# Performance work log

Hardware: AMD Instinct MI355X
Metric: run time of the kernel (lower is better)

## Reference

```python
import jax, jax.numpy as jnp
import numpy as np

B, L, D, W = 4, 512, 768, 12
K = L * W  # number of candidate spans


def _mlp(x, w1, b1, w2, b2):
    # Linear -> ReLU -> (Dropout=identity in eval) -> Linear
    return jax.nn.relu(x @ w1.T + b1) @ w2.T + b2


def setup_inputs() -> dict:
    key = jax.random.key(0)
    ks = jax.random.split(key, 16)
    sc_d = 1.0 / np.sqrt(D)
    sc_4d = 1.0 / np.sqrt(4 * D)
    sc_2d = 1.0 / np.sqrt(2 * D)
    inp = {
        "h": jax.random.normal(ks[0], (B, L, D), dtype=jnp.float32),
        "span_idx": jax.random.randint(ks[1], (B, K, 2), 0, L, dtype=jnp.int64),
        # project_start: Linear(D,4D), Linear(4D,D)
        "ws1": jax.random.uniform(ks[2], (4 * D, D), jnp.float32, -sc_d, sc_d),
        "bs1": jax.random.uniform(ks[3], (4 * D,), jnp.float32, -sc_d, sc_d),
        "ws2": jax.random.uniform(ks[4], (D, 4 * D), jnp.float32, -sc_4d, sc_4d),
        "bs2": jax.random.uniform(ks[5], (D,), jnp.float32, -sc_4d, sc_4d),
        # project_end
        "we1": jax.random.uniform(ks[6], (4 * D, D), jnp.float32, -sc_d, sc_d),
        "be1": jax.random.uniform(ks[7], (4 * D,), jnp.float32, -sc_d, sc_d),
        "we2": jax.random.uniform(ks[8], (D, 4 * D), jnp.float32, -sc_4d, sc_4d),
        "be2": jax.random.uniform(ks[9], (D,), jnp.float32, -sc_4d, sc_4d),
        # out_project: Linear(2D,4D), Linear(4D,D)
        "wo1": jax.random.uniform(ks[10], (4 * D, 2 * D), jnp.float32, -sc_2d, sc_2d),
        "bo1": jax.random.uniform(ks[11], (4 * D,), jnp.float32, -sc_2d, sc_2d),
        "wo2": jax.random.uniform(ks[12], (D, 4 * D), jnp.float32, -sc_4d, sc_4d),
        "bo2": jax.random.uniform(ks[13], (D,), jnp.float32, -sc_4d, sc_4d),
    }
    return inp


def reference(h, span_idx, ws1, bs1, ws2, bs2, we1, be1, we2, be2, wo1, bo1, wo2, bo2):
    start_rep = _mlp(h, ws1, bs1, ws2, bs2)  # [B, L, D]
    end_rep = _mlp(h, we1, be1, we2, be2)    # [B, L, D]
    bidx = jnp.arange(B)[:, None]
    start_span = start_rep[bidx, span_idx[:, :, 0]]  # gather along seq dim -> [B, K, D]
    end_span = end_rep[bidx, span_idx[:, :, 1]]      # [B, K, D]
    cat = jax.nn.relu(jnp.concatenate([start_span, end_span], axis=-1))  # [B, K, 2D]
    out = _mlp(cat, wo1, bo1, wo2, bo2)  # [B, K, D]
    return out.reshape(B, L, W, D)
```

## Files before the change

### kernel.cpp

```cpp
#include <hip/hip_runtime.h>
#include <hip/hip_bf16.h>

using bf16 = __hip_bfloat16;
using bf16x8 = __attribute__((ext_vector_type(8))) __bf16;
using f32x4  = __attribute__((ext_vector_type(4))) float;
typedef unsigned short ushort_t;

#define BM 128
#define BN 128
#define BK 32


__device__ __forceinline__ void gl_lds16(const void* g, void* l) {
  __builtin_amdgcn_global_load_lds(
      (const __attribute__((address_space(1))) void*)g,
      (__attribute__((address_space(3))) void*)l, 16, 0, 0);
}

__device__ __forceinline__ ushort_t f2bf(float f) {
  unsigned u = __float_as_uint(f);
  u += 0x7FFF + ((u >> 16) & 1);
  return (ushort_t)(u >> 16);
}

__global__ void sniff(const unsigned* __restrict__ w1,
                      const unsigned* __restrict__ idx, int* flags) {
  __shared__ int cnt[2];
  if (threadIdx.x == 0) { cnt[0] = 0; cnt[1] = 0; }
  __syncthreads();
  int t = threadIdx.x;
  int c0 = 0;
  for (int k = 0; k < 4; ++k) {
    unsigned lo = w1[t * 4 + k] & 0xFFFFu;
    unsigned e = (lo >> 7) & 0xFF;
    if (e <= 122) c0++;
  }
  int c1 = (idx[2 * t + 1] != 0) ? 1 : 0;
  atomicAdd(&cnt[0], c0);
  atomicAdd(&cnt[1], c1);
  __syncthreads();
  if (threadIdx.x == 0) {
    flags[0] = (cnt[0] >= 900) ? 1 : 0;
    flags[1] = (cnt[1] == 0) ? 1 : 0;
  }
}

__global__ void norm_idx(const int* __restrict__ flags, const void* __restrict__ src,
                         int* __restrict__ dst) {
  int i = blockIdx.x * 256 + threadIdx.x;
  int v = flags[1] ? (int)((const long long*)src)[i] : ((const int*)src)[i];
  dst[i] = v;
}

__global__ void cvt_all(const int* __restrict__ flags,
                        const void* s0, const void* s1, const void* s2,
                        const void* s3, const void* s4, const void* s5,
                        const void* s6, ushort_t* __restrict__ dst) {
  long i = ((long)blockIdx.x * 256 + threadIdx.x) * 4;
  const void* src; long off;
  if      (i <  1572864) { src = s0; off = i; }
  else if (i <  3932160) { src = s1; off = i - 1572864; }
  else if (i <  6291456) { src = s2; off = i - 3932160; }
  else if (i <  8650752) { src = s3; off = i - 6291456; }
  else if (i < 11010048) { src = s4; off = i - 8650752; }
  else if (i < 15728640) { src = s5; off = i - 11010048; }
  else                   { src = s6; off = i - 15728640; }
  if (flags[0]) {
    *(ushort4*)(dst + i) = *((const ushort4*)((const ushort_t*)src + off));
  } else {
    float4 f = ((const float4*)src)[off >> 2];
    ushort4 o;
    o.x = f2bf(f.x); o.y = f2bf(f.y); o.z = f2bf(f.z); o.w = f2bf(f.w);
    *(ushort4*)(dst + i) = o;
  }
}

__global__ void cvt_bias(const int* __restrict__ flags,
                         const void* b0, const void* b1, const void* b2,
                         const void* b3, const void* b4, const void* b5,
                         float* __restrict__ dst) {
  int i = blockIdx.x * 256 + threadIdx.x;
  if (i >= 14592) return;
  if (i >= 11520) { dst[i] = 0.f; return; }
  const void* src; int off;
  if (i < 3072)       { src = b0; off = i; }
  else if (i < 3840)  { src = b1; off = i - 3072; }
  else if (i < 6912)  { src = b2; off = i - 3840; }
  else if (i < 7680)  { src = b3; off = i - 6912; }
  else if (i < 10752) { src = b4; off = i - 7680; }
  else                { src = b5; off = i - 10752; }
  dst[i] = flags[0] ? __bfloat162float(((const bf16*)src)[off])
                    : ((const float*)src)[off];
}

template <bool GATHER, bool RELU, bool OUTF32>
__global__ __launch_bounds__(256) void gemm_bt(
    const bf16* __restrict__ A, const bf16* __restrict__ A2,
    const bf16* __restrict__ repS, const bf16* __restrict__ repE,
    const int* __restrict__ sidx, int row_base,
    const bf16* __restrict__ Bw, const bf16* __restrict__ Bw2,
    const float* __restrict__ bias, const float* __restrict__ bias2,
    void* __restrict__ C, void* __restrict__ C2, int nsplit,
    int N, int Kdim, int bstride) {
  __shared__ bf16 lA[BM * BK];
  __shared__ bf16 lB[BN * BK];

  const int tid  = threadIdx.x;
  const int lane = tid & 63;
  const int wave = tid >> 6;
  const int wm = wave >> 1, wn = wave & 1;
  int by = blockIdx.y;
  const bf16* Bw_ = Bw; const float* bias_ = bias; void* C_ = C; const bf16* A_ = A;
  if (by >= nsplit) { by -= nsplit; Bw_ = Bw2; bias_ = bias2; C_ = C2; A_ = A2; }
  const int m0 = blockIdx.x * BM;
  const int n0 = by * BN;

  const int srow = tid >> 2;
  const int scol = 8 * ((tid & 3) ^ ((tid >> 3) & 3));

  const bf16 *a0 = nullptr, *a1 = nullptr;
  const bf16 *pS0 = nullptr, *pE0 = nullptr, *pS1 = nullptr, *pE1 = nullptr;
  if (GATHER) {
    int r0 = row_base + m0 + srow;
    int r1 = r0 + 64;
    int b0 = r0 / 6144, b1 = r1 / 6144;
    int s0 = min(max(sidx[2 * r0], 0), 511);
    int e0 = min(max(sidx[2 * r0 + 1], 0), 511);
    int s1 = min(max(sidx[2 * r1], 0), 511);
    int e1 = min(max(sidx[2 * r1 + 1], 0), 511);
    pS0 = repS + ((size_t)b0 * 512 + s0) * 768 + scol;
    pE0 = repE + ((size_t)b0 * 512 + e0) * 768 + scol;
    pS1 = repS + ((size_t)b1 * 512 + s1) * 768 + scol;
    pE1 = repE + ((size_t)b1 * 512 + e1) * 768 + scol;
  } else {
    a0 = A_ + (size_t)(m0 + srow) * Kdim + scol;
    a1 = a0 + (size_t)64 * Kdim;
  }
  const bf16* b0p = Bw_ + (size_t)(n0 + srow) * bstride + scol;
  const bf16* b1p = b0p + (size_t)64 * bstride;

  f32x4 acc[4][4];
  const f32x4 z = {0.f, 0.f, 0.f, 0.f};
#pragma unroll
  for (int i = 0; i < 4; ++i)
#pragma unroll
    for (int j = 0; j < 4; ++j) acc[i][j] = z;

  const int fr = lane & 15;
  const int fk = 8 * ((lane >> 4) ^ ((lane >> 1) & 3));

  for (int k0 = 0; k0 < Kdim; k0 += BK) {
    const bf16 *sa0, *sa1;
    if (GATHER) {
      if (k0 < 768) { sa0 = pS0 + k0; sa1 = pS1 + k0; }
      else          { sa0 = pE0 + (k0 - 768); sa1 = pE1 + (k0 - 768); }
    } else {
      sa0 = a0 + k0; sa1 = a1 + k0;
    }
    gl_lds16(sa0, lA + tid * 8);
    gl_lds16(sa1, lA + 2048 + tid * 8);
    gl_lds16(b0p + k0, lB + tid * 8);
    gl_lds16(b1p + k0, lB + 2048 + tid * 8);
    __syncthreads();

    bf16x8 af[4], bv[4];
#pragma unroll
    for (int i = 0; i < 4; ++i)
      af[i] = *(const bf16x8*)(const void*)(lA + (wm * 64 + i * 16 + fr) * BK + fk);
#pragma unroll
    for (int j = 0; j < 4; ++j)
      bv[j] = *(const bf16x8*)(const void*)(lB + (wn * 64 + j * 16 + fr) * BK + fk);
#pragma unroll
    for (int i = 0; i < 4; ++i)
#pragma unroll
      for (int j = 0; j < 4; ++j)
        acc[i][j] = __builtin_amdgcn_mfma_f32_16x16x32_bf16(af[i], bv[j], acc[i][j], 0, 0, 0);
    __syncthreads();
  }

  float* Cf = (float*)C_;
  bf16*  Cb = (bf16*)C_;
#pragma unroll
  for (int j = 0; j < 4; ++j) {
    int n = n0 + wn * 64 + j * 16 + fr;
    float bj = bias_[n];
#pragma unroll
    for (int i = 0; i < 4; ++i) {
      int mb = m0 + wm * 64 + i * 16 + (lane >> 4) * 4;
#pragma unroll
      for (int r = 0; r < 4; ++r) {
        float v = acc[i][j][r] + bj;
        if (RELU) v = fmaxf(v, 0.f);
        if (OUTF32) Cf[(size_t)(mb + r) * N + n] = v;
        else        Cb[(size_t)(mb + r) * N + n] = __float2bfloat16(v);
      }
    }
  }
}

#define FM 64
#define FN 128
__global__ __launch_bounds__(256) void gemm_final_fused(
    const ushort_t* __restrict__ Ps, const ushort_t* __restrict__ Pe,
    const int* __restrict__ sidx,
    const bf16* __restrict__ Bw, const float* __restrict__ bias,
    float* __restrict__ out) {
  __shared__ bf16 lA[2 * 2048];
  __shared__ bf16 lB[2 * 4096];

  const int tid  = threadIdx.x;
  const int lane = tid & 63;
  const int wave = tid >> 6;
  const int wm = wave >> 1, wn = wave & 1;
  const int m0 = blockIdx.x * FM;
  const int n0 = blockIdx.y * FN;

  const int srow = tid >> 2;
  const int scol = 8 * ((tid & 3) ^ ((tid >> 3) & 3));

  int r0 = m0 + srow;
  int b0 = r0 / 6144;
  int s0 = min(max(sidx[2 * r0], 0), 511);
  int e0 = min(max(sidx[2 * r0 + 1], 0), 511);
  const ushort_t* pS0 = Ps + ((size_t)b0 * 512 + s0) * 3072 + scol;
  const ushort_t* pE0 = Pe + ((size_t)b0 * 512 + e0) * 3072 + scol;

  const bf16* bp0 = Bw + (size_t)(n0 + srow) * 3072 + scol;
  const bf16* bp1 = bp0 + (size_t)64 * 3072;

  f32x4 acc[2][4];
  const f32x4 z = {0.f, 0.f, 0.f, 0.f};
#pragma unroll
  for (int i = 0; i < 2; ++i)
#pragma unroll
    for (int j = 0; j < 4; ++j) acc[i][j] = z;

  const int fr = lane & 15;
  const int fk = 8 * ((lane >> 4) ^ ((lane >> 1) & 3));

  auto pack_store = [&](uint4 xs, uint4 xe, bf16* dst) {
    unsigned w[4];
    const unsigned* us = &xs.x;
    const unsigned* ue = &xe.x;
#pragma unroll
    for (int q = 0; q < 4; ++q) {
      float lo = fmaxf(__uint_as_float(us[q] << 16) + __uint_as_float(ue[q] << 16), 0.f);
      float hi = fmaxf(__uint_as_float(us[q] & 0xFFFF0000u) +
                       __uint_as_float(ue[q] & 0xFFFF0000u), 0.f);
      asm("v_cvt_pk_bf16_f32 %0, %1, %2" : "=v"(w[q]) : "v"(lo), "v"(hi));
    }
    *(uint4*)(void*)dst = *(const uint4*)w;
  };

  {
    gl_lds16(bp0, lB + tid * 8);
    gl_lds16(bp1, lB + 2048 + tid * 8);
    uint4 xs0 = *(const uint4*)(const void*)pS0;
    uint4 xe0 = *(const uint4*)(const void*)pE0;
    pack_store(xs0, xe0, lA + tid * 8);
    __syncthreads();
  }

  for (int it = 0; it < 96; ++it) {
    const int curA = (it & 1) << 11;
    const int curB = (it & 1) << 12;
    const int nxtA = ((it + 1) & 1) << 11;
    const int nxtB = ((it + 1) & 1) << 12;
    const int k1 = (it + 1) * BK;
    const bool pre = (it + 1) < 96;
    uint4 xs0, xe0;
    if (pre) {
      gl_lds16(bp0 + k1, lB + nxtB + tid * 8);
      gl_lds16(bp1 + k1, lB + nxtB + 2048 + tid * 8);
      xs0 = *(const uint4*)(const void*)(pS0 + k1);
      xe0 = *(const uint4*)(const void*)(pE0 + k1);
    }

    bf16x8 af[2];
#pragma unroll
    for (int i = 0; i < 2; ++i)
      af[i] = *(const bf16x8*)(const void*)(lA + curA + (wm * 32 + i * 16 + fr) * BK + fk);
#pragma unroll
    for (int j = 0; j < 4; ++j) {
      bf16x8 bv = *(const bf16x8*)(const void*)(lB + curB + (wn * 64 + j * 16 + fr) * BK + fk);
#pragma unroll
      for (int i = 0; i < 2; ++i)
        acc[i][j] = __builtin_amdgcn_mfma_f32_16x16x32_bf16(af[i], bv, acc[i][j], 0, 0, 0);
    }

    if (pre) {
      pack_store(xs0, xe0, lA + nxtA + tid * 8);
    }
    __syncthreads();
  }

#pragma unroll
  for (int j = 0; j < 4; ++j) {
    int n = n0 + wn * 64 + j * 16 + fr;
    float bj = bias[n];
#pragma unroll
    for (int i = 0; i < 2; ++i) {
      int mb = m0 + wm * 32 + i * 16 + (lane >> 4) * 4;
#pragma unroll
      for (int r = 0; r < 4; ++r)
        out[(size_t)(mb + r) * 768 + n] = acc[i][j][r] + bj;
    }
  }
}

extern "C" void kernel_launch(void* const* d_in, const int* in_sizes, int n_in,
                              void* d_out, int out_size, void* d_ws, size_t ws_size,
                              hipStream_t stream) {
  const void* h    = d_in[0];
  const void* sidx = d_in[1];
  const void *ws1 = d_in[2],  *bs1 = d_in[3];
  const void *ws2 = d_in[4],  *bs2 = d_in[5];
  const void *we1 = d_in[6],  *be1 = d_in[7];
  const void *we2 = d_in[8],  *be2 = d_in[9];
  const void *wo1 = d_in[10], *bo1 = d_in[11];
  const void *wo2 = d_in[12], *bo2 = d_in[13];

  char* p = (char*)d_ws;
  int*      flags = (int*)p;
  int*      idx32 = (int*)(p + 256);
  float*    biasf = (float*)(p + 256 + 196608);
  ushort_t* hb    = (ushort_t*)(p + 256 + 196608 + 65536);
  ushort_t* w1sb  = hb   + (size_t)1572864;
  ushort_t* w2sb  = w1sb + (size_t)2359296;
  ushort_t* w1eb  = w2sb + (size_t)2359296;
  ushort_t* w2eb  = w1eb + (size_t)2359296;
  ushort_t* wo1b  = w2eb + (size_t)2359296;
  ushort_t* wo2b  = wo1b + (size_t)4718592;
  ushort_t* repS  = wo2b + (size_t)2359296;
  ushort_t* repE  = repS + (size_t)1572864;
  char*     R     = (char*)(repE + (size_t)1572864);
  size_t fixed = (size_t)(R - (char*)d_ws);
  if (ws_size < fixed) return;
  size_t Rsz = ws_size - fixed;

  const size_t P_BF = (size_t)2 * 2048 * 3072 * 2;
  int tier = (Rsz >= P_BF) ? 2 : 3;

  dim3 blk(256);
  const int XBIG = 0x40000000;
  sniff<<<1, blk, 0, stream>>>((const unsigned*)ws1, (const unsigned*)sidx, flags);
  norm_idx<<<192, blk, 0, stream>>>(flags, sidx, idx32);
  cvt_all<<<17664, blk, 0, stream>>>(flags, h, ws1, ws2, we1, we2, wo1, wo2, hb);
  cvt_bias<<<57, blk, 0, stream>>>(flags, bs1, bs2, be1, be2, bo1, bo2, biasf);
  const float *bs1f = biasf, *bs2f = biasf + 3072, *be1f = biasf + 3840,
              *be2f = biasf + 6912, *bo1f = biasf + 7680, *bo2f = biasf + 10752,
              *zerof = biasf + 11520;
  float* outf = (float*)d_out;

  if (tier == 2) {
    ushort_t* hidS = (ushort_t*)R;
    ushort_t* hidE = hidS + (size_t)2048 * 3072;
    gemm_bt<false, true, false><<<dim3(16, 48), blk, 0, stream>>>(
        (const bf16*)hb, (const bf16*)hb, nullptr, nullptr, nullptr, 0,
        (const bf16*)w1sb, (const bf16*)w1eb, bs1f, be1f,
        hidS, hidE, 24, 3072, 768, 768);
    gemm_bt<false, true, false><<<dim3(16, 12), blk, 0, stream>>>(
        (const bf16*)hidS, (const bf16*)hidE, nullptr, nullptr, nullptr, 0,
        (const bf16*)w2sb, (const bf16*)w2eb, bs2f, be2f,
        (bf16*)repS, (bf16*)repE, 6, 768, 3072, 3072);
    ushort_t* Ps = (ushort_t*)R;
    ushort_t* Pe = Ps + (size_t)2048 * 3072;
    gemm_bt<false, false, false><<<dim3(16, 48), blk, 0, stream>>>(
        (const bf16*)repS, (const bf16*)repE, nullptr, nullptr, nullptr, 0,
        (const bf16*)wo1b, (const bf16*)wo1b + 768, bo1f, zerof,
        Ps, Pe, 24, 3072, 768, 1536);
    gemm_final_fused<<<dim3(384, 6), blk, 0, stream>>>(
        Ps, Pe, idx32, (const bf16*)wo2b, bo2f, outf);
  } else {
    long long cT = (long long)(Rsz / ((size_t)2 * 3072 * 2));
    cT = (cT / 128) * 128; if (cT > 2048) cT = 2048;
    long long cO = (long long)(Rsz / ((size_t)3072 * 2));
    cO = (cO / 128) * 128; if (cO > 24576) cO = 24576;
    if (cT < 128 || cO < 128) return;
    ushort_t* scr = (ushort_t*)R;
    for (long long r = 0; r < 2048; r += cT) {
      long long mc = 2048 - r < cT ? 2048 - r : cT;
      ushort_t* hidS = scr;
      ushort_t* hidE = scr + (size_t)cT * 3072;
      gemm_bt<false, true, false><<<dim3(mc / 128, 48), blk, 0, stream>>>(
          (const bf16*)hb + r * 768, (const bf16*)hb + r * 768,
          nullptr, nullptr, nullptr, 0,
          (const bf16*)w1sb, (const bf16*)w1eb, bs1f, be1f,
          hidS, hidE, 24, 3072, 768, 768);
      gemm_bt<false, true, false><<<dim3(mc / 128, 12), blk, 0, stream>>>(
          (const bf16*)hidS, (const bf16*)hidE, nullptr, nullptr, nullptr, 0,
          (const bf16*)w2sb, (const bf16*)w2eb, bs2f, be2f,
          (bf16*)repS + r * 768, (bf16*)repE + r * 768, 6, 768, 3072, 3072);
    }
    for (long long r = 0; r < 24576; r += cO) {
      long long mc = 24576 - r < cO ? 24576 - r : cO;
      gemm_bt<true, true, false><<<dim3(mc / 128, 24), blk, 0, stream>>>(
          nullptr, nullptr, (const bf16*)repS, (const bf16*)repE, idx32, (int)r,
          (const bf16*)wo1b, nullptr, bo1f, nullptr,
          scr, nullptr, XBIG, 3072, 1536, 1536);
      gemm_bt<false, false, true><<<dim3(mc / 128, 6), blk, 0, stream>>>(
          (const bf16*)scr, nullptr, nullptr, nullptr, nullptr, 0,
          (const bf16*)wo2b, nullptr, bo2f, nullptr,
          outf + (size_t)r * 768, nullptr, XBIG, 768, 3072, 3072);
    }
  }
}
```

Measured before the change: 562.6 us.

## Deepen A-operand prefetch to two stages with explicit waitcnt scheduling

Restructures the final out-projection GEMM main loop so the gathered start/end span rows are loaded two K-steps ahead in registers, while the weight tile is still loaded one step ahead via global_load_lds. Scheduling barriers and manual vmcnt/lgkmcnt waits replace __syncthreads. This lets the gather latency overlap more MFMA work instead of stalling. It costs extra registers for the second prefetch buffer, and the hand-written wait counts depend on the exact issue order, so the pipeline is fragile.

```diff
diff --git a/kernel.cpp b/kernel.cpp
--- a/kernel.cpp
+++ b/kernel.cpp
@@ -4,6 +4,7 @@
 using bf16 = __hip_bfloat16;
 using bf16x8 = __attribute__((ext_vector_type(8))) __bf16;
 using f32x4  = __attribute__((ext_vector_type(4))) float;
+using u32x4  = __attribute__((ext_vector_type(4))) unsigned;
 typedef unsigned short ushort_t;
 
 #define BM 128
@@ -16,6 +17,10 @@
       (const __attribute__((address_space(1))) void*)g,
       (__attribute__((address_space(3))) void*)l, 16, 0, 0);
 }
+
+#define SB0() __builtin_amdgcn_sched_barrier(0)
+#define WAITV(n) asm volatile("s_waitcnt vmcnt(" #n ")" ::: "memory")
+#define WAITL() asm volatile("s_waitcnt lgkmcnt(0)" ::: "memory")
 
 __device__ __forceinline__ ushort_t f2bf(float f) {
   unsigned u = __float_as_uint(f);
@@ -238,61 +243,93 @@
   const int fr = lane & 15;
   const int fk = 8 * ((lane >> 4) ^ ((lane >> 1) & 3));
 
-  auto pack_store = [&](uint4 xs, uint4 xe, bf16* dst) {
-    unsigned w[4];
-    const unsigned* us = &xs.x;
-    const unsigned* ue = &xe.x;
+  auto pack_store = [&](u32x4 xs, u32x4 xe, bf16* dst) {
+    u32x4 wv;
 #pragma unroll
     for (int q = 0; q < 4; ++q) {
-      float lo = fmaxf(__uint_as_float(us[q] << 16) + __uint_as_float(ue[q] << 16), 0.f);
-      float hi = fmaxf(__uint_as_float(us[q] & 0xFFFF0000u) +
-                       __uint_as_float(ue[q] & 0xFFFF0000u), 0.f);
-      asm("v_cvt_pk_bf16_f32 %0, %1, %2" : "=v"(w[q]) : "v"(lo), "v"(hi));
-    }
-    *(uint4*)(void*)dst = *(const uint4*)w;
+      float lo = fmaxf(__uint_as_float(xs[q] << 16) + __uint_as_float(xe[q] << 16), 0.f);
+      float hi = fmaxf(__uint_as_float(xs[q] & 0xFFFF0000u) +
+                       __uint_as_float(xe[q] & 0xFFFF0000u), 0.f);
+      unsigned w;
+      asm("v_cvt_pk_bf16_f32 %0, %1, %2" : "=v"(w) : "v"(lo), "v"(hi));
+      wv[q] = w;
+    }
+    *(u32x4*)(void*)dst = wv;
   };
 
-  {
-    gl_lds16(bp0, lB + tid * 8);
-    gl_lds16(bp1, lB + 2048 + tid * 8);
-    uint4 xs0 = *(const uint4*)(const void*)pS0;
-    uint4 xe0 = *(const uint4*)(const void*)pE0;
-    pack_store(xs0, xe0, lA + tid * 8);
-    __syncthreads();
-  }
-
-  for (int it = 0; it < 96; ++it) {
-    const int curA = (it & 1) << 11;
-    const int curB = (it & 1) << 12;
-    const int nxtA = ((it + 1) & 1) << 11;
-    const int nxtB = ((it + 1) & 1) << 12;
-    const int k1 = (it + 1) * BK;
-    const bool pre = (it + 1) < 96;
-    uint4 xs0, xe0;
-    if (pre) {
-      gl_lds16(bp0 + k1, lB + nxtB + tid * 8);
-      gl_lds16(bp1 + k1, lB + nxtB + 2048 + tid * 8);
-      xs0 = *(const uint4*)(const void*)(pS0 + k1);
-      xe0 = *(const uint4*)(const void*)(pE0 + k1);
-    }
-
+  auto mfma_tile = [&](int cA, int cB) {
     bf16x8 af[2];
 #pragma unroll
     for (int i = 0; i < 2; ++i)
-      af[i] = *(const bf16x8*)(const void*)(lA + curA + (wm * 32 + i * 16 + fr) * BK + fk);
+      af[i] = *(const bf16x8*)(const void*)(lA + cA + (wm * 32 + i * 16 + fr) * BK + fk);
 #pragma unroll
     for (int j = 0; j < 4; ++j) {
-      bf16x8 bv = *(const bf16x8*)(const void*)(lB + curB + (wn * 64 + j * 16 + fr) * BK + fk);
+      bf16x8 bv = *(const bf16x8*)(const void*)(lB + cB + (wn * 64 + j * 16 + fr) * BK + fk);
 #pragma unroll
       for (int i = 0; i < 2; ++i)
         acc[i][j] = __builtin_amdgcn_mfma_f32_16x16x32_bf16(af[i], bv, acc[i][j], 0, 0, 0);
     }
-
-    if (pre) {
-      pack_store(xs0, xe0, lA + nxtA + tid * 8);
-    }
-    __syncthreads();
-  }
+  };
+
+  u32x4 xs0, xe0, xs1, xe1;
+
+  xs0 = *(const u32x4*)(const void*)pS0;
+  xe0 = *(const u32x4*)(const void*)pE0;
+  SB0();
+  gl_lds16(bp0, lB + tid * 8);
+  gl_lds16(bp1, lB + 2048 + tid * 8);
+  SB0();
+  xs1 = *(const u32x4*)(const void*)(pS0 + 32);
+  xe1 = *(const u32x4*)(const void*)(pE0 + 32);
+  SB0();
+  pack_store(xs0, xe0, lA + tid * 8);
+  WAITV(2);
+  WAITL();
+  SB0();
+  __builtin_amdgcn_s_barrier();
+  SB0();
+
+  auto kstep = [&](int t, u32x4& sPk, u32x4& ePk, u32x4& sLd, u32x4& eLd) {
+    const int cA = (t & 1) << 11, cB = (t & 1) << 12;
+    const int nA = cA ^ 2048,     nB = cB ^ 4096;
+    const int kB = (t + 1) * BK;
+    const int kA = (t + 2) * BK;
+    gl_lds16(bp0 + kB, lB + nB + tid * 8);
+    gl_lds16(bp1 + kB, lB + nB + 2048 + tid * 8);
+    SB0();
+    sLd = *(const u32x4*)(const void*)(pS0 + kA);
+    eLd = *(const u32x4*)(const void*)(pE0 + kA);
+    SB0();
+
+    mfma_tile(cA, cB);
+
+    pack_store(sPk, ePk, lA + nA + tid * 8);
+    WAITV(2);
+    WAITL();
+    SB0();
+    __builtin_amdgcn_s_barrier();
+    SB0();
+  };
+
+  for (int m = 0; m < 47; ++m) {
+    kstep(2 * m,     xs1, xe1, xs0, xe0);
+    kstep(2 * m + 1, xs0, xe0, xs1, xe1);
+  }
+
+  {
+    gl_lds16(bp0 + 95 * BK, lB + 4096 + tid * 8);
+    gl_lds16(bp1 + 95 * BK, lB + 4096 + 2048 + tid * 8);
+    SB0();
+    mfma_tile(0, 0);
+    pack_store(xs1, xe1, lA + 2048 + tid * 8);
+    WAITV(0);
+    WAITL();
+    SB0();
+    __builtin_amdgcn_s_barrier();
+    SB0();
+  }
+
+  mfma_tile(2048, 4096);
 
 #pragma unroll
   for (int j = 0; j < 4; ++j) {
```

New measurement: 557.2 us. Within noise of the previous version (-1.0%).

## Widen final fused GEMM tile to 64x384 with 8 waves to cut gather redundancy

Applied to the files above, without the earlier changes.

The final gather+GEMM kernel now uses 512-thread blocks, each computing a 64x384 output tile instead of 64x128. The grid shrinks from 6 to 2 column blocks. Each gathered Ps/Pe row pair is then loaded and ReLU-packed only twice instead of six times, which cuts redundant gather traffic and ALU work. The cost is a larger LDS footprint for B (about 48KB double-buffered), half the threads idle during A packing, and fewer blocks in flight per CU.

```diff
diff --git a/kernel.cpp b/kernel.cpp
--- a/kernel.cpp
+++ b/kernel.cpp
@@ -4,6 +4,7 @@
 using bf16 = __hip_bfloat16;
 using bf16x8 = __attribute__((ext_vector_type(8))) __bf16;
 using f32x4  = __attribute__((ext_vector_type(4))) float;
+using u32x4  = __attribute__((ext_vector_type(4))) unsigned;
 typedef unsigned short ushort_t;
 
 #define BM 128
@@ -198,109 +199,117 @@
   }
 }
 
-#define FM 64
-#define FN 128
-__global__ __launch_bounds__(256) void gemm_final_fused(
+__global__ __launch_bounds__(512) void gemm_final_fused(
     const ushort_t* __restrict__ Ps, const ushort_t* __restrict__ Pe,
     const int* __restrict__ sidx,
     const bf16* __restrict__ Bw, const float* __restrict__ bias,
     float* __restrict__ out) {
   __shared__ bf16 lA[2 * 2048];
-  __shared__ bf16 lB[2 * 4096];
+  __shared__ bf16 lB[2 * 12288];
 
   const int tid  = threadIdx.x;
   const int lane = tid & 63;
   const int wave = tid >> 6;
-  const int wm = wave >> 1, wn = wave & 1;
-  const int m0 = blockIdx.x * FM;
-  const int n0 = blockIdx.y * FN;
+  const int m0 = blockIdx.x * 64;
+  const int n0 = blockIdx.y * 384;
 
   const int srow = tid >> 2;
   const int scol = 8 * ((tid & 3) ^ ((tid >> 3) & 3));
 
-  int r0 = m0 + srow;
-  int b0 = r0 / 6144;
-  int s0 = min(max(sidx[2 * r0], 0), 511);
-  int e0 = min(max(sidx[2 * r0 + 1], 0), 511);
-  const ushort_t* pS0 = Ps + ((size_t)b0 * 512 + s0) * 3072 + scol;
-  const ushort_t* pE0 = Pe + ((size_t)b0 * 512 + e0) * 3072 + scol;
-
-  const bf16* bp0 = Bw + (size_t)(n0 + srow) * 3072 + scol;
-  const bf16* bp1 = bp0 + (size_t)64 * 3072;
-
-  f32x4 acc[2][4];
+  const ushort_t *pS0 = nullptr, *pE0 = nullptr;
+  if (tid < 256) {
+    int r0 = m0 + srow;
+    int b0 = r0 / 6144;
+    int s0 = min(max(sidx[2 * r0], 0), 511);
+    int e0 = min(max(sidx[2 * r0 + 1], 0), 511);
+    pS0 = Ps + ((size_t)b0 * 512 + s0) * 3072 + scol;
+    pE0 = Pe + ((size_t)b0 * 512 + e0) * 3072 + scol;
+  }
+  const bf16* bp0 = Bw + (size_t)(n0 +       srow) * 3072 + scol;
+  const bf16* bp1 = Bw + (size_t)(n0 + 128 + srow) * 3072 + scol;
+  const bf16* bp2 = Bw + (size_t)(n0 + 256 + srow) * 3072 + scol;
+
+  f32x4 acc[4][3];
   const f32x4 z = {0.f, 0.f, 0.f, 0.f};
 #pragma unroll
-  for (int i = 0; i < 2; ++i)
-#pragma unroll
-    for (int j = 0; j < 4; ++j) acc[i][j] = z;
+  for (int i = 0; i < 4; ++i)
+#pragma unroll
+    for (int j = 0; j < 3; ++j) acc[i][j] = z;
 
   const int fr = lane & 15;
   const int fk = 8 * ((lane >> 4) ^ ((lane >> 1) & 3));
 
-  auto pack_store = [&](uint4 xs, uint4 xe, bf16* dst) {
-    unsigned w[4];
-    const unsigned* us = &xs.x;
-    const unsigned* ue = &xe.x;
+  auto pack_store = [&](u32x4 xs, u32x4 xe, bf16* dst) {
+    u32x4 wv;
 #pragma unroll
     for (int q = 0; q < 4; ++q) {
-      float lo = fmaxf(__uint_as_float(us[q] << 16) + __uint_as_float(ue[q] << 16), 0.f);
-      float hi = fmaxf(__uint_as_float(us[q] & 0xFFFF0000u) +
-                       __uint_as_float(ue[q] & 0xFFFF0000u), 0.f);
-      asm("v_cvt_pk_bf16_f32 %0, %1, %2" : "=v"(w[q]) : "v"(lo), "v"(hi));
-    }
-    *(uint4*)(void*)dst = *(const uint4*)w;
+      float lo = fmaxf(__uint_as_float(xs[q] << 16) + __uint_as_float(xe[q] << 16), 0.f);
+      float hi = fmaxf(__uint_as_float(xs[q] & 0xFFFF0000u) +
+                       __uint_as_float(xe[q] & 0xFFFF0000u), 0.f);
+      unsigned w;
+      asm("v_cvt_pk_bf16_f32 %0, %1, %2" : "=v"(w) : "v"(lo), "v"(hi));
+      wv[q] = w;
+    }
+    *(u32x4*)(void*)dst = wv;
   };
 
   {
     gl_lds16(bp0, lB + tid * 8);
-    gl_lds16(bp1, lB + 2048 + tid * 8);
-    uint4 xs0 = *(const uint4*)(const void*)pS0;
-    uint4 xe0 = *(const uint4*)(const void*)pE0;
-    pack_store(xs0, xe0, lA + tid * 8);
+    gl_lds16(bp1, lB + 4096 + tid * 8);
+    gl_lds16(bp2, lB + 8192 + tid * 8);
+    if (tid < 256) {
+      u32x4 xs = *(const u32x4*)(const void*)pS0;
+      u32x4 xe = *(const u32x4*)(const void*)pE0;
+      pack_store(xs, xe, lA + tid * 8);
+    }
     __syncthreads();
   }
 
   for (int it = 0; it < 96; ++it) {
     const int curA = (it & 1) << 11;
-    const int curB = (it & 1) << 12;
-    const int nxtA = ((it + 1) & 1) << 11;
-    const int nxtB = ((it + 1) & 1) << 12;
+    const int curB = (it & 1) * 12288;
+    const int nxtA = curA ^ 2048;
+    const int nxtB = (curB == 0) ? 12288 : 0;
     const int k1 = (it + 1) * BK;
     const bool pre = (it + 1) < 96;
-    uint4 xs0, xe0;
+    u32x4 xs, xe;
     if (pre) {
       gl_lds16(bp0 + k1, lB + nxtB + tid * 8);
-      gl_lds16(bp1 + k1, lB + nxtB + 2048 + tid * 8);
-      xs0 = *(const uint4*)(const void*)(pS0 + k1);
-      xe0 = *(const uint4*)(const void*)(pE0 + k1);
-    }
-
-    bf16x8 af[2];
-#pragma unroll
-    for (int i = 0; i < 2; ++i)
-      af[i] = *(const bf16x8*)(const void*)(lA + curA + (wm * 32 + i * 16 + fr) * BK + fk);
-#pragma unroll
-    for (int j = 0; j < 4; ++j) {
-      bf16x8 bv = *(const bf16x8*)(const void*)(lB + curB + (wn * 64 + j * 16 + fr) * BK + fk);
-#pragma unroll
-      for (int i = 0; i < 2; ++i)
+      gl_lds16(bp1 + k1, lB + nxtB + 4096 + tid * 8);
+      gl_lds16(bp2 + k1, lB + nxtB + 8192 + tid * 8);
+      if (tid < 256) {
+        xs = *(const u32x4*)(const void*)(pS0 + k1);
+        xe = *(const u32x4*)(const void*)(pE0 + k1);
+      }
+    }
+
+    bf16x8 af[4];
+#pragma unroll
+    for (int i = 0; i < 4; ++i)
+      af[i] = *(const bf16x8*)(const void*)(lA + curA + (i * 16 + fr) * BK + fk);
+#pragma unroll
+    for (int j = 0; j < 3; ++j) {
+      const int nb = wave * 48 + j * 16;
+      bf16x8 bv = *(const bf16x8*)(const void*)(
+          lB + curB + (nb >> 7) * 4096 + ((nb & 127) + fr) * BK + fk);
+#pragma unroll
+      for (int i = 0; i < 4; ++i)
         acc[i][j] = __builtin_amdgcn_mfma_f32_16x16x32_bf16(af[i], bv, acc[i][j], 0, 0, 0);
     }
 
-    if (pre) {
-      pack_store(xs0, xe0, lA + nxtA + tid * 8);
+    if (pre && tid < 256) {
+      pack_store(xs, xe, lA + nxtA + tid * 8);
     }
     __syncthreads();
   }
 
 #pragma unroll
-  for (int j = 0; j < 4; ++j) {
-    int n = n0 + wn * 64 + j * 16 + fr;
+  for (int j = 0; j < 3; ++j) {
+    int n = n0 + wave * 48 + j * 16 + fr;
     float bj = bias[n];
 #pragma unroll
-    for (int i = 0; i < 2; ++i) {
-      int mb = m0 + wm * 32 + i * 16 + (lane >> 4) * 4;
+    for (int i = 0; i < 4; ++i) {
+      int mb = m0 + i * 16 + (lane >> 4) * 4;
 #pragma unroll
       for (int r = 0; r < 4; ++r)
         out[(size_t)(mb + r) * 768 + n] = acc[i][j][r] + bj;
@@ -369,7 +378,7 @@
         (const bf16*)repS, (const bf16*)repE, nullptr, nullptr, nullptr, 0,
         (const bf16*)wo1b, (const bf16*)wo1b + 768, bo1f, zerof,
         Ps, Pe, 24, 3072, 768, 1536);
-    gemm_final_fused<<<dim3(384, 6), blk, 0, stream>>>(
+    gemm_final_fused<<<dim3(384, 2), dim3(512), 0, stream>>>(
         Ps, Pe, idx32, (const bf16*)wo2b, bo2f, outf);
   } else {
     long long cT = (long long)(Rsz / ((size_t)2 * 3072 * 2));
```

New measurement: 485.4 us. 1.16x faster.
